# Performance work log

Measured on AMD Instinct MI355X. Metric: run time of the kernel, lower is better.

Reference implementation:

```python
import jax, jax.numpy as jnp
import numpy as np

N_ENT = 100000
N_REL = 200          # -> 2*N_REL = 400 edge types
D = 128
NB = 4               # num_bases (hard-coded in MGCN)
E = 800000


def _rgcn_conv(x, src, dst, edge_type, edge_norm, basis, att, root, bias):
    # x: [N, D]; basis: [NB, D, D]; att: [2R, NB]; root: [D, D]; bias: [D]
    n = x.shape[0]
    x_j = x[src]                      # [E, D] gather source node feats
    att_e = att[edge_type]            # [E, NB] per-edge basis coefficients
    # message: x_j @ (sum_b att_e[b] * basis_b), computed basis-wise to avoid
    # materializing [E, D, D] per-edge weights (same math as gather+bmm)
    msg = att_e[:, 0:1] * (x_j @ basis[0])
    for b in range(1, NB):
        msg = msg + att_e[:, b:b+1] * (x_j @ basis[b])
    msg = msg * edge_norm[:, None]
    # mean aggregation into target nodes (zeros for isolated nodes)
    agg = jax.ops.segment_sum(msg, dst, num_segments=n)
    cnt = jax.ops.segment_sum(jnp.ones_like(edge_norm), dst, num_segments=n)
    agg = agg / jnp.maximum(cnt, 1.0)[:, None]
    return agg + x @ root + bias


def setup_inputs() -> dict:
    key = jax.random.key(0)
    ks = jax.random.split(key, 16)
    s = 1.0 / np.sqrt(NB * D)  # uniform init scale as in reset_parameters
    inp = {
        "entity": jnp.arange(N_ENT, dtype=jnp.int32),
        "edge_index": jax.random.randint(ks[0], (2, E), 0, N_ENT, dtype=jnp.int32),
        "edge_type": jax.random.randint(ks[1], (E,), 0, 2 * N_REL, dtype=jnp.int32),
        "edge_norm": jax.random.uniform(ks[2], (E,), dtype=jnp.float32),
        "emb": jax.random.normal(ks[3], (N_ENT, D), dtype=jnp.float32),
        "basis1": jax.random.uniform(ks[4], (NB, D, D), dtype=jnp.float32, minval=-s, maxval=s),
        "att1": jax.random.uniform(ks[5], (2 * N_REL, NB), dtype=jnp.float32, minval=-s, maxval=s),
        "root1": jax.random.uniform(ks[6], (D, D), dtype=jnp.float32, minval=-s, maxval=s),
        "bias1": jax.random.uniform(ks[7], (D,), dtype=jnp.float32, minval=-s, maxval=s),
        "basis2": jax.random.uniform(ks[8], (NB, D, D), dtype=jnp.float32, minval=-s, maxval=s),
        "att2": jax.random.uniform(ks[9], (2 * N_REL, NB), dtype=jnp.float32, minval=-s, maxval=s),
        "root2": jax.random.uniform(ks[10], (D, D), dtype=jnp.float32, minval=-s, maxval=s),
        "bias2": jax.random.uniform(ks[11], (D,), dtype=jnp.float32, minval=-s, maxval=s),
    }
    return inp


def reference(entity, edge_index, edge_type, edge_norm, emb,
              basis1, att1, root1, bias1, basis2, att2, root2, bias2):
    src, dst = edge_index[0], edge_index[1]
    x = emb[entity]  # [N, D]
    # forward applies conv1 TWICE (as in the original code), then conv2;
    # dropout is identity in eval mode
    x = _rgcn_conv(x, src, dst, edge_type, edge_norm, basis1, att1, root1, bias1)
    x = jax.nn.relu(_rgcn_conv(x, src, dst, edge_type, edge_norm, basis1, att1, root1, bias1))
    x = _rgcn_conv(x, src, dst, edge_type, edge_norm, basis2, att2, root2, bias2)
    return x
```

## Files before the change

kernel.cpp:

```cpp
#include <hip/hip_runtime.h>

#define D 128
#define NB 4
#define BM2 256
#define SCAN_B 1024
#define FILL_PASSES 4

typedef unsigned short u16;
typedef unsigned int u32;
using bf16x8 = __attribute__((ext_vector_type(8))) short;
using f32x4  = __attribute__((ext_vector_type(4))) float;

__device__ __forceinline__ float bf2f(u16 u) {
    union { u32 i; float f; } v; v.i = ((u32)u) << 16; return v.f;
}
__device__ __forceinline__ u16 f2bf(float f) {
    union { float ff; u32 i; } v; v.ff = f;
    u32 r = v.i + 0x7fffu + ((v.i >> 16) & 1u);
    return (u16)(r >> 16);
}

__device__ __forceinline__ void async16(void* lds, const void* g) {
    __builtin_amdgcn_global_load_lds(
        (const __attribute__((address_space(1))) unsigned int*)g,
        (__attribute__((address_space(3))) unsigned int*)lds,
        16, 0, 0);
}


__global__ __launch_bounds__(256) void degree_int_kernel(const int* __restrict__ dst,
                                                         int* __restrict__ deg, int E) {
    int e = blockIdx.x * 256 + threadIdx.x;
    if (e < E) atomicAdd(&deg[dst[e]], 1);
}

__global__ __launch_bounds__(256) void scan1_kernel(const int* __restrict__ deg,
                                                    int* __restrict__ row_start,
                                                    int* __restrict__ bsum, int n) {
    __shared__ int tsum[256];
    int base = blockIdx.x * SCAN_B;
    int t = threadIdx.x;
    int v[4];
    int s = 0;
#pragma unroll
    for (int i = 0; i < 4; ++i) {
        int idx = base + t * 4 + i;
        v[i] = (idx < n) ? deg[idx] : 0;
        s += v[i];
    }
    tsum[t] = s;
    __syncthreads();
    for (int off = 1; off < 256; off <<= 1) {
        int x = (t >= off) ? tsum[t - off] : 0;
        __syncthreads();
        tsum[t] += x;
        __syncthreads();
    }
    int run = tsum[t] - s;
#pragma unroll
    for (int i = 0; i < 4; ++i) {
        int idx = base + t * 4 + i;
        if (idx < n) row_start[idx] = run;
        run += v[i];
    }
    if (t == 255) bsum[blockIdx.x] = tsum[255];
}

__global__ __launch_bounds__(256) void scan2_kernel(int* __restrict__ bsum, int nb) {
    __shared__ int buf[256];
    __shared__ int carry_s;
    if (threadIdx.x == 0) carry_s = 0;
    __syncthreads();
    for (int base = 0; base < nb; base += 256) {
        int i = base + threadIdx.x;
        int v = (i < nb) ? bsum[i] : 0;
        buf[threadIdx.x] = v;
        __syncthreads();
        for (int off = 1; off < 256; off <<= 1) {
            int x = (threadIdx.x >= (unsigned)off) ? buf[threadIdx.x - off] : 0;
            __syncthreads();
            buf[threadIdx.x] += x;
            __syncthreads();
        }
        if (i < nb) bsum[i] = carry_s + buf[threadIdx.x] - v;
        __syncthreads();
        if (threadIdx.x == 0) carry_s += buf[255];
        __syncthreads();
    }
}

__global__ __launch_bounds__(256) void scan3_kernel(const int* __restrict__ deg,
                                                    const int* __restrict__ bsum,
                                                    int* __restrict__ row_start,
                                                    float* __restrict__ inv, int n, int E) {
    int i = blockIdx.x * 256 + threadIdx.x;
    if (i < n) {
        row_start[i] += bsum[i >> 10];
        inv[i] = 1.0f / fmaxf((float)deg[i], 1.0f);
    }
    if (i == 0) row_start[n] = E;
}

__global__ __launch_bounds__(256) void fill_kernel(
    const int* __restrict__ src, const int* __restrict__ dst,
    const int* __restrict__ row_start, int* __restrict__ fill,
    int2* __restrict__ csr_se, int E, int nchunks, int chunk)
{
    int b = blockIdx.x;
    int p = b / nchunks;
    int e = (b % nchunks) * 256 + threadIdx.x;
    if (e >= E) return;
    int d0 = dst[e];
    int lo = p * chunk;
    if (d0 < lo || d0 >= lo + chunk) return;
    int pos = row_start[d0] + atomicAdd(&fill[d0], 1);
    csr_se[pos] = make_int2(src[e], e);
}

__global__ __launch_bounds__(256) void coef_kernel(
    const int2* __restrict__ csr_se, const int* __restrict__ etype,
    const float* __restrict__ norm, const float* __restrict__ att,
    float4* __restrict__ csr_coef, int E)
{
    int p = blockIdx.x * 256 + threadIdx.x;
    if (p >= E) return;
    int e = csr_se[p].y;
    float nm = norm[e];
    float4 a = ((const float4*)att)[etype[e]];
    csr_coef[p] = make_float4(a.x * nm, a.y * nm, a.z * nm, a.w * nm);
}


__global__ __launch_bounds__(256) void tobf_gather_kernel(const int* __restrict__ entity,
                                                          const float* __restrict__ emb,
                                                          u16* __restrict__ xbf, int n) {
    int idx = blockIdx.x * 256 + threadIdx.x;
    if (idx >= n * 32) return;
    int row = idx >> 5, c = idx & 31;
    float4 v = ((const float4*)emb)[(size_t)entity[row] * 32 + c];
    ushort4 o;
    o.x = f2bf(v.x); o.y = f2bf(v.y); o.z = f2bf(v.z); o.w = f2bf(v.w);
    ((ushort4*)xbf)[idx] = o;
}

#define AGG_BODY(UJ)                                                            \
    {                                                                           \
        float4 c = c_[UJ];                                                      \
        float4 xv;                                                              \
        xv.x = bf2f(u_[UJ].x); xv.y = bf2f(u_[UJ].y);                           \
        xv.z = bf2f(u_[UJ].z); xv.w = bf2f(u_[UJ].w);                           \
        z0.x += c.x * xv.x; z0.y += c.x * xv.y; z0.z += c.x * xv.z; z0.w += c.x * xv.w; \
        z1.x += c.y * xv.x; z1.y += c.y * xv.y; z1.z += c.y * xv.z; z1.w += c.y * xv.w; \
        z2.x += c.z * xv.x; z2.y += c.z * xv.y; z2.z += c.z * xv.z; z2.w += c.z * xv.w; \
        z3.x += c.w * xv.x; z3.y += c.w * xv.y; z3.z += c.w * xv.z; z3.w += c.w * xv.w; \
    }

__global__ __launch_bounds__(256) void agg_kernel(
    const int* __restrict__ row_start, const int* __restrict__ deg,
    const float* __restrict__ inv, const int2* __restrict__ csr_se,
    const float4* __restrict__ csr_coef, const u16* __restrict__ xbf,
    u16* __restrict__ Zbf, int n)
{
    int nd = blockIdx.x * 8 + (threadIdx.x >> 5);
    if (nd >= n) return;
    int q = threadIdx.x & 31;
    int s0 = row_start[nd];
    int dg = deg[nd];
    float4 z0 = make_float4(0.f,0.f,0.f,0.f), z1 = z0, z2 = z0, z3 = z0;

    int i = 0;
    for (; i + 8 <= dg; i += 8) {
        int s_[8]; float4 c_[8]; ushort4 u_[8];
#pragma unroll
        for (int j = 0; j < 8; ++j) s_[j] = csr_se[s0 + i + j].x;
#pragma unroll
        for (int j = 0; j < 8; ++j) c_[j] = csr_coef[s0 + i + j];
#pragma unroll
        for (int j = 0; j < 8; ++j) u_[j] = ((const ushort4*)xbf)[(size_t)s_[j] * 32 + q];
#pragma unroll
        for (int j = 0; j < 8; ++j) AGG_BODY(j)
    }
    for (; i + 4 <= dg; i += 4) {
        int s_[4]; float4 c_[4]; ushort4 u_[4];
#pragma unroll
        for (int j = 0; j < 4; ++j) s_[j] = csr_se[s0 + i + j].x;
#pragma unroll
        for (int j = 0; j < 4; ++j) c_[j] = csr_coef[s0 + i + j];
#pragma unroll
        for (int j = 0; j < 4; ++j) u_[j] = ((const ushort4*)xbf)[(size_t)s_[j] * 32 + q];
#pragma unroll
        for (int j = 0; j < 4; ++j) AGG_BODY(j)
    }
    for (; i < dg; ++i) {
        int s_[1]; float4 c_[1]; ushort4 u_[1];
        s_[0] = csr_se[s0 + i].x;
        c_[0] = csr_coef[s0 + i];
        u_[0] = ((const ushort4*)xbf)[(size_t)s_[0] * 32 + q];
        AGG_BODY(0)
    }

    float iv = inv[nd];
    ushort4* zp = ((ushort4*)Zbf) + (size_t)nd * 128;
    ushort4 o;
    o.x = f2bf(z0.x * iv); o.y = f2bf(z0.y * iv); o.z = f2bf(z0.z * iv); o.w = f2bf(z0.w * iv);
    zp[q] = o;
    o.x = f2bf(z1.x * iv); o.y = f2bf(z1.y * iv); o.z = f2bf(z1.z * iv); o.w = f2bf(z1.w * iv);
    zp[32 + q] = o;
    o.x = f2bf(z2.x * iv); o.y = f2bf(z2.y * iv); o.z = f2bf(z2.z * iv); o.w = f2bf(z2.w * iv);
    zp[64 + q] = o;
    o.x = f2bf(z3.x * iv); o.y = f2bf(z3.y * iv); o.z = f2bf(z3.z * iv); o.w = f2bf(z3.w * iv);
    zp[96 + q] = o;
}

__global__ __launch_bounds__(256) void wprep_kernel(
    const float* __restrict__ basis, const float* __restrict__ root,
    u16* __restrict__ Wt)
{
    int idx = blockIdx.x * 256 + threadIdx.x;
    if (idx >= 640 * 128) return;
    int k = idx >> 7, nn = idx & 127;
    float w = (k < 512) ? basis[(size_t)k * 128 + nn] : root[(size_t)(k - 512) * 128 + nn];
    u16 hi = f2bf(w);
    float lo = w - bf2f(hi);
    Wt[(size_t)nn * 1280 + k] = hi;
    Wt[(size_t)nn * 1280 + 640 + k] = f2bf(lo);
}

__global__ __launch_bounds__(512) void mfma_gemm_kernel(
    const u16* __restrict__ Zbf, const u16* __restrict__ xbf,
    const u16* __restrict__ Wt, const float* __restrict__ bias,
    int relu, int write_bf, u16* __restrict__ obf, float* __restrict__ of32, int n)
{
    __shared__ u16 As[BM2 * 64];
    __shared__ u16 Bs[128 * 64];

    const int tid  = threadIdx.x;
    const int row0 = blockIdx.x * BM2;
    const int lane = tid & 63;
    const int w    = tid >> 6;
    const int wr   = (w >> 1) * 64;
    const int wc   = (w & 1) * 64;
    const int lr   = lane & 15;
    const int lk   = lane >> 4;

    const int srow = lane >> 3;
    const int sswz = ((lane & 7) * 16) ^ (srow << 4);

    f32x4 zero = {0.f, 0.f, 0.f, 0.f};
    f32x4 acc[4][4];
#pragma unroll
    for (int mi = 0; mi < 4; ++mi)
#pragma unroll
        for (int ni = 0; ni < 4; ++ni) acc[mi][ni] = zero;

    for (int s = 0; s < 20; ++s) {
        const int ac = s >> 1;
        const int wk = (s & 1) * 640 + ac * 64;
        __syncthreads();
        if ((s & 1) == 0) {
#pragma unroll
            for (int j = 0; j < 4; ++j) {
                int r    = (w << 5) + (j << 3) + srow;
                int grow = row0 + r;
                const u16* gp = (ac < 8)
                    ? (Zbf + (size_t)grow * 512 + ac * 64)
                    : (xbf + (size_t)grow * 128 + (ac - 8) * 64);
                async16((char*)As + (((w << 5) + (j << 3)) << 7),
                        (const char*)gp + sswz);
            }
        }
#pragma unroll
        for (int j = 0; j < 2; ++j) {
            int rr = (w << 4) + (j << 3) + srow;
            const u16* gp = Wt + (size_t)rr * 1280 + wk;
            async16((char*)Bs + (((w << 4) + (j << 3)) << 7),
                    (const char*)gp + sswz);
        }
        __syncthreads();

#pragma unroll
        for (int kh = 0; kh < 2; ++kh) {
            const int kb = (kh * 64 + lk * 16) ^ ((lr & 7) << 4);
            bf16x8 af[4], bfr[4];
#pragma unroll
            for (int mi = 0; mi < 4; ++mi)
                af[mi] = *(const bf16x8*)((const char*)As + ((wr + mi * 16 + lr) << 7) + kb);
#pragma unroll
            for (int ni = 0; ni < 4; ++ni)
                bfr[ni] = *(const bf16x8*)((const char*)Bs + ((wc + ni * 16 + lr) << 7) + kb);
#pragma unroll
            for (int mi = 0; mi < 4; ++mi)
#pragma unroll
                for (int ni = 0; ni < 4; ++ni)
                    acc[mi][ni] = __builtin_amdgcn_mfma_f32_16x16x32_bf16(
                        af[mi], bfr[ni], acc[mi][ni], 0, 0, 0);
        }
    }

#pragma unroll
    for (int ni = 0; ni < 4; ++ni) {
        int col = wc + ni * 16 + lr;
        float bv = bias[col];
#pragma unroll
        for (int mi = 0; mi < 4; ++mi) {
#pragma unroll
            for (int r = 0; r < 4; ++r) {
                int row = row0 + wr + mi * 16 + lk * 4 + r;
                if (row < n) {
                    float v = acc[mi][ni][r] + bv;
                    if (relu) v = fmaxf(v, 0.f);
                    if (write_bf) obf[(size_t)row * 128 + col] = f2bf(v);
                    else          of32[(size_t)row * 128 + col] = v;
                }
            }
        }
    }
}


extern "C" void kernel_launch(void* const* d_in, const int* in_sizes, int n_in,
                              void* d_out, int out_size, void* d_ws, size_t ws_size,
                              hipStream_t stream) {
    const int*   entity     = (const int*)d_in[0];
    const int*   edge_index = (const int*)d_in[1];
    const int*   edge_type  = (const int*)d_in[2];
    const float* edge_norm  = (const float*)d_in[3];
    const float* emb        = (const float*)d_in[4];
    const float* basis1     = (const float*)d_in[5];
    const float* att1       = (const float*)d_in[6];
    const float* root1      = (const float*)d_in[7];
    const float* bias1      = (const float*)d_in[8];
    const float* basis2     = (const float*)d_in[9];
    const float* att2       = (const float*)d_in[10];
    const float* root2      = (const float*)d_in[11];
    const float* bias2      = (const float*)d_in[12];
    float* out = (float*)d_out;

    const int N = in_sizes[0];
    const int E = in_sizes[2];
    const int* src = edge_index;
    const int* dst = edge_index + E;

    size_t ND = (size_t)N * D;
    char* wp = (char*)d_ws;
    int nb = (N + SCAN_B - 1) / SCAN_B;

    size_t off = 0;
    u16*    Zbf      = (u16*)(wp + off);   off += ND * 8;
    u16*    xbf0     = (u16*)(wp + off);   off += ND * 2;
    u16*    Wt       = (u16*)(wp + off);   off += (size_t)128 * 1280 * 2;
    float4* csr_coef = (float4*)(wp + off); off += (size_t)E * 16;
    int2*   csr_se   = (int2*)(wp + off);  off += (size_t)E * 8;
    int*    deg      = (int*)(wp + off);   off += (size_t)N * 4;
    int*    fill     = (int*)(wp + off);   off += (size_t)N * 4;
    float*  inv      = (float*)(wp + off); off += (size_t)N * 4;
    int*    row_start= (int*)(wp + off);   off += (size_t)(N + 1) * 4;
    int*    bsum     = (int*)(wp + off);   off += (size_t)(nb + 1) * 4;
    size_t need = off;

    if (ws_size < need) {
        hipMemsetAsync(d_out, 0, (size_t)out_size * sizeof(float), stream);
        return;
    }

    u16* xbf1 = (u16*)d_out;

    int eblk = (E + 255) / 256;
    int ablk = (N + 7) / 8;
    int gblk = (N * 32 + 255) / 256;
    int mblk = (N + BM2 - 1) / BM2;
    int wblk = (640 * 128 + 255) / 256;
    int nblk256 = (N + 255) / 256;
    int chunk = (N + FILL_PASSES - 1) / FILL_PASSES;

    hipMemsetAsync(deg, 0, (size_t)N * 4, stream);
    degree_int_kernel<<<eblk, 256, 0, stream>>>(dst, deg, E);
    scan1_kernel<<<nb, 256, 0, stream>>>(deg, row_start, bsum, N);
    scan2_kernel<<<1, 256, 0, stream>>>(bsum, nb);
    scan3_kernel<<<nblk256, 256, 0, stream>>>(deg, bsum, row_start, inv, N, E);
    hipMemsetAsync(fill, 0, (size_t)N * 4, stream);
    fill_kernel<<<eblk * FILL_PASSES, 256, 0, stream>>>(src, dst, row_start, fill,
                                                        csr_se, E, eblk, chunk);
    coef_kernel<<<eblk, 256, 0, stream>>>(csr_se, edge_type, edge_norm, att1, csr_coef, E);
    tobf_gather_kernel<<<gblk, 256, 0, stream>>>(entity, emb, xbf0, N);
    wprep_kernel<<<wblk, 256, 0, stream>>>(basis1, root1, Wt);

    agg_kernel<<<ablk, 256, 0, stream>>>(row_start, deg, inv, csr_se, csr_coef, xbf0, Zbf, N);
    mfma_gemm_kernel<<<mblk, 512, 0, stream>>>(Zbf, xbf0, Wt, bias1, 0, 1, xbf1, nullptr, N);

    agg_kernel<<<ablk, 256, 0, stream>>>(row_start, deg, inv, csr_se, csr_coef, xbf1, Zbf, N);
    mfma_gemm_kernel<<<mblk, 512, 0, stream>>>(Zbf, xbf1, Wt, bias1, 1, 1, xbf0, nullptr, N);

    coef_kernel<<<eblk, 256, 0, stream>>>(csr_se, edge_type, edge_norm, att2, csr_coef, E);
    wprep_kernel<<<wblk, 256, 0, stream>>>(basis2, root2, Wt);
    agg_kernel<<<ablk, 256, 0, stream>>>(row_start, deg, inv, csr_se, csr_coef, xbf0, Zbf, N);
    mfma_gemm_kernel<<<mblk, 512, 0, stream>>>(Zbf, xbf0, Wt, bias2, 0, 0, nullptr, out, N);
}
```

Measured before the change: 460.9 us.

## Fuse per-edge coefficient computation into aggregation and simplify CSR build

Removes the coef_kernel and its per-edge float4 coefficient buffer. The aggregation kernel now gathers edge_type and edge_norm through the stored edge id and computes att*norm inline, and it derives degree from row_start. The CSR fill now uses a device-to-device copy of row_start as the atomic cursor instead of a memset plus separate add. The degree kernel is also split into dst-range passes like the fill kernel. In exchange, each aggregation pass adds random gathers of etype, norm and att per edge, three times over.

```diff
diff --git a/kernel.cpp b/kernel.cpp
--- a/kernel.cpp
+++ b/kernel.cpp
@@ -28,10 +28,18 @@
 }
 
 
-__global__ __launch_bounds__(256) void degree_int_kernel(const int* __restrict__ dst,
-                                                         int* __restrict__ deg, int E) {
-    int e = blockIdx.x * 256 + threadIdx.x;
-    if (e < E) atomicAdd(&deg[dst[e]], 1);
+__global__ __launch_bounds__(256) void degree_int_kernel(
+    const int* __restrict__ dst, int* __restrict__ deg,
+    int E, int nchunks, int chunk)
+{
+    int b = blockIdx.x;
+    int p = b / nchunks;
+    int e = (b % nchunks) * 256 + threadIdx.x;
+    if (e >= E) return;
+    int d0 = dst[e];
+    int lo = p * chunk;
+    if (d0 < lo || d0 >= lo + chunk) return;
+    atomicAdd(&deg[d0], 1);
 }
 
 __global__ __launch_bounds__(256) void scan1_kernel(const int* __restrict__ deg,
@@ -103,8 +111,8 @@
 
 __global__ __launch_bounds__(256) void fill_kernel(
     const int* __restrict__ src, const int* __restrict__ dst,
-    const int* __restrict__ row_start, int* __restrict__ fill,
-    int2* __restrict__ csr_se, int E, int nchunks, int chunk)
+    int* __restrict__ fillpos, int2* __restrict__ csr_se,
+    int E, int nchunks, int chunk)
 {
     int b = blockIdx.x;
     int p = b / nchunks;
@@ -113,21 +121,8 @@
     int d0 = dst[e];
     int lo = p * chunk;
     if (d0 < lo || d0 >= lo + chunk) return;
-    int pos = row_start[d0] + atomicAdd(&fill[d0], 1);
+    int pos = atomicAdd(&fillpos[d0], 1);
     csr_se[pos] = make_int2(src[e], e);
-}
-
-__global__ __launch_bounds__(256) void coef_kernel(
-    const int2* __restrict__ csr_se, const int* __restrict__ etype,
-    const float* __restrict__ norm, const float* __restrict__ att,
-    float4* __restrict__ csr_coef, int E)
-{
-    int p = blockIdx.x * 256 + threadIdx.x;
-    if (p >= E) return;
-    int e = csr_se[p].y;
-    float nm = norm[e];
-    float4 a = ((const float4*)att)[etype[e]];
-    csr_coef[p] = make_float4(a.x * nm, a.y * nm, a.z * nm, a.w * nm);
 }
 
 
@@ -145,7 +140,9 @@
 
 #define AGG_BODY(UJ)                                                            \
     {                                                                           \
-        float4 c = c_[UJ];                                                      \
+        float4 c = ((const float4*)att)[t_[UJ]];                                \
+        float nm = nm_[UJ];                                                     \
+        c.x *= nm; c.y *= nm; c.z *= nm; c.w *= nm;                             \
         float4 xv;                                                              \
         xv.x = bf2f(u_[UJ].x); xv.y = bf2f(u_[UJ].y);                           \
         xv.z = bf2f(u_[UJ].z); xv.w = bf2f(u_[UJ].w);                           \
@@ -156,46 +153,51 @@
     }
 
 __global__ __launch_bounds__(256) void agg_kernel(
-    const int* __restrict__ row_start, const int* __restrict__ deg,
-    const float* __restrict__ inv, const int2* __restrict__ csr_se,
-    const float4* __restrict__ csr_coef, const u16* __restrict__ xbf,
-    u16* __restrict__ Zbf, int n)
+    const int* __restrict__ row_start, const float* __restrict__ inv,
+    const int2* __restrict__ csr_se, const int* __restrict__ etype,
+    const float* __restrict__ norm, const float* __restrict__ att,
+    const u16* __restrict__ xbf, u16* __restrict__ Zbf, int n)
 {
     int nd = blockIdx.x * 8 + (threadIdx.x >> 5);
     if (nd >= n) return;
     int q = threadIdx.x & 31;
     int s0 = row_start[nd];
-    int dg = deg[nd];
+    int dg = row_start[nd + 1] - s0;
     float4 z0 = make_float4(0.f,0.f,0.f,0.f), z1 = z0, z2 = z0, z3 = z0;
 
     int i = 0;
     for (; i + 8 <= dg; i += 8) {
-        int s_[8]; float4 c_[8]; ushort4 u_[8];
-#pragma unroll
-        for (int j = 0; j < 8; ++j) s_[j] = csr_se[s0 + i + j].x;
-#pragma unroll
-        for (int j = 0; j < 8; ++j) c_[j] = csr_coef[s0 + i + j];
-#pragma unroll
-        for (int j = 0; j < 8; ++j) u_[j] = ((const ushort4*)xbf)[(size_t)s_[j] * 32 + q];
+        int2 se_[8]; int t_[8]; float nm_[8]; ushort4 u_[8];
+#pragma unroll
+        for (int j = 0; j < 8; ++j) se_[j] = csr_se[s0 + i + j];
+#pragma unroll
+        for (int j = 0; j < 8; ++j) t_[j] = etype[se_[j].y];
+#pragma unroll
+        for (int j = 0; j < 8; ++j) nm_[j] = norm[se_[j].y];
+#pragma unroll
+        for (int j = 0; j < 8; ++j) u_[j] = ((const ushort4*)xbf)[(size_t)se_[j].x * 32 + q];
 #pragma unroll
         for (int j = 0; j < 8; ++j) AGG_BODY(j)
     }
     for (; i + 4 <= dg; i += 4) {
-        int s_[4]; float4 c_[4]; ushort4 u_[4];
-#pragma unroll
-        for (int j = 0; j < 4; ++j) s_[j] = csr_se[s0 + i + j].x;
-#pragma unroll
-        for (int j = 0; j < 4; ++j) c_[j] = csr_coef[s0 + i + j];
-#pragma unroll
-        for (int j = 0; j < 4; ++j) u_[j] = ((const ushort4*)xbf)[(size_t)s_[j] * 32 + q];
+        int2 se_[4]; int t_[4]; float nm_[4]; ushort4 u_[4];
+#pragma unroll
+        for (int j = 0; j < 4; ++j) se_[j] = csr_se[s0 + i + j];
+#pragma unroll
+        for (int j = 0; j < 4; ++j) t_[j] = etype[se_[j].y];
+#pragma unroll
+        for (int j = 0; j < 4; ++j) nm_[j] = norm[se_[j].y];
+#pragma unroll
+        for (int j = 0; j < 4; ++j) u_[j] = ((const ushort4*)xbf)[(size_t)se_[j].x * 32 + q];
 #pragma unroll
         for (int j = 0; j < 4; ++j) AGG_BODY(j)
     }
     for (; i < dg; ++i) {
-        int s_[1]; float4 c_[1]; ushort4 u_[1];
-        s_[0] = csr_se[s0 + i].x;
-        c_[0] = csr_coef[s0 + i];
-        u_[0] = ((const ushort4*)xbf)[(size_t)s_[0] * 32 + q];
+        int2 se_[1]; int t_[1]; float nm_[1]; ushort4 u_[1];
+        se_[0] = csr_se[s0 + i];
+        t_[0] = etype[se_[0].y];
+        nm_[0] = norm[se_[0].y];
+        u_[0] = ((const ushort4*)xbf)[(size_t)se_[0].x * 32 + q];
         AGG_BODY(0)
     }
 
@@ -349,10 +351,9 @@
     u16*    Zbf      = (u16*)(wp + off);   off += ND * 8;
     u16*    xbf0     = (u16*)(wp + off);   off += ND * 2;
     u16*    Wt       = (u16*)(wp + off);   off += (size_t)128 * 1280 * 2;
-    float4* csr_coef = (float4*)(wp + off); off += (size_t)E * 16;
     int2*   csr_se   = (int2*)(wp + off);  off += (size_t)E * 8;
     int*    deg      = (int*)(wp + off);   off += (size_t)N * 4;
-    int*    fill     = (int*)(wp + off);   off += (size_t)N * 4;
+    int*    fillpos  = (int*)(wp + off);   off += (size_t)N * 4;
     float*  inv      = (float*)(wp + off); off += (size_t)N * 4;
     int*    row_start= (int*)(wp + off);   off += (size_t)(N + 1) * 4;
     int*    bsum     = (int*)(wp + off);   off += (size_t)(nb + 1) * 4;
@@ -374,25 +375,26 @@
     int chunk = (N + FILL_PASSES - 1) / FILL_PASSES;
 
     hipMemsetAsync(deg, 0, (size_t)N * 4, stream);
-    degree_int_kernel<<<eblk, 256, 0, stream>>>(dst, deg, E);
+    degree_int_kernel<<<eblk * FILL_PASSES, 256, 0, stream>>>(dst, deg, E, eblk, chunk);
     scan1_kernel<<<nb, 256, 0, stream>>>(deg, row_start, bsum, N);
     scan2_kernel<<<1, 256, 0, stream>>>(bsum, nb);
     scan3_kernel<<<nblk256, 256, 0, stream>>>(deg, bsum, row_start, inv, N, E);
-    hipMemsetAsync(fill, 0, (size_t)N * 4, stream);
-    fill_kernel<<<eblk * FILL_PASSES, 256, 0, stream>>>(src, dst, row_start, fill,
-                                                        csr_se, E, eblk, chunk);
-    coef_kernel<<<eblk, 256, 0, stream>>>(csr_se, edge_type, edge_norm, att1, csr_coef, E);
+    hipMemcpyAsync(fillpos, row_start, (size_t)N * 4, hipMemcpyDeviceToDevice, stream);
+    fill_kernel<<<eblk * FILL_PASSES, 256, 0, stream>>>(src, dst, fillpos, csr_se,
+                                                        E, eblk, chunk);
     tobf_gather_kernel<<<gblk, 256, 0, stream>>>(entity, emb, xbf0, N);
     wprep_kernel<<<wblk, 256, 0, stream>>>(basis1, root1, Wt);
 
-    agg_kernel<<<ablk, 256, 0, stream>>>(row_start, deg, inv, csr_se, csr_coef, xbf0, Zbf, N);
+    agg_kernel<<<ablk, 256, 0, stream>>>(row_start, inv, csr_se, edge_type, edge_norm,
+                                         att1, xbf0, Zbf, N);
     mfma_gemm_kernel<<<mblk, 512, 0, stream>>>(Zbf, xbf0, Wt, bias1, 0, 1, xbf1, nullptr, N);
 
-    agg_kernel<<<ablk, 256, 0, stream>>>(row_start, deg, inv, csr_se, csr_coef, xbf1, Zbf, N);
+    agg_kernel<<<ablk, 256, 0, stream>>>(row_start, inv, csr_se, edge_type, edge_norm,
+                                         att1, xbf1, Zbf, N);
     mfma_gemm_kernel<<<mblk, 512, 0, stream>>>(Zbf, xbf1, Wt, bias1, 1, 1, xbf0, nullptr, N);
 
-    coef_kernel<<<eblk, 256, 0, stream>>>(csr_se, edge_type, edge_norm, att2, csr_coef, E);
     wprep_kernel<<<wblk, 256, 0, stream>>>(basis2, root2, Wt);
-    agg_kernel<<<ablk, 256, 0, stream>>>(row_start, deg, inv, csr_se, csr_coef, xbf0, Zbf, N);
+    agg_kernel<<<ablk, 256, 0, stream>>>(row_start, inv, csr_se, edge_type, edge_norm,
+                                         att2, xbf0, Zbf, N);
     mfma_gemm_kernel<<<mblk, 512, 0, stream>>>(Zbf, xbf0, Wt, bias2, 0, 0, nullptr, out, N);
 }
```

Result: slower. 554.8 us (+20.4%).
